# Kernel tuning notes

Hardware: AMD Instinct MI355X
Metric: run time of the kernel (lower is better)

The kernel has to match this reference:

```python
import jax, jax.numpy as jnp
import numpy as np
import math

NTOKEN = 32000; D = 512; H = 8; DFF = 2048; L = 4; B = 4; S = 1024; EPS = 1e-5


def _ln(x, g, b):
    m = x.mean(-1, keepdims=True)
    v = ((x - m) ** 2).mean(-1, keepdims=True)
    return (x - m) * jax.lax.rsqrt(v + EPS) * g + b


def setup_inputs() -> dict:
    key = jax.random.key(0)
    ks = jax.random.split(key, 20)
    s = 0.02
    rn = lambda k, shape: jax.random.normal(k, shape, jnp.float32) * s
    return {
        "src": jax.random.randint(ks[0], (B, S), 0, NTOKEN, jnp.int32),
        "emb": rn(ks[1], (NTOKEN, D)),
        "conv_w": rn(ks[2], (D, 1, 3)), "conv_b": rn(ks[3], (D,)),
        "bn_g": jnp.ones((D,)), "bn_b": jnp.zeros((D,)),
        "bn_m": jnp.zeros((D,)), "bn_v": jnp.ones((D,)),
        "w_ih": rn(ks[4], (4 * D, D)), "w_hh": rn(ks[5], (4 * D, D)),
        "b_ih": rn(ks[6], (4 * D,)), "b_hh": rn(ks[7], (4 * D,)),
        "in_w": rn(ks[8], (L, 3 * D, D)), "in_b": rn(ks[9], (L, 3 * D)),
        "out_w": rn(ks[10], (L, D, D)), "out_b": rn(ks[11], (L, D)),
        "ln1_g": jnp.ones((L, D)), "ln1_b": jnp.zeros((L, D)),
        "w1": rn(ks[12], (L, DFF, D)), "b1": rn(ks[13], (L, DFF)),
        "w2": rn(ks[14], (L, D, DFF)), "b2": rn(ks[15], (L, D)),
        "ln2_g": jnp.ones((L, D)), "ln2_b": jnp.zeros((L, D)),
        "fin_g": jnp.ones((D,)), "fin_b": jnp.zeros((D,)),
    }


def _forward(src, emb, conv_w, conv_b, bn_g, bn_b, bn_m, bn_v,
             w_ih, w_hh, b_ih, b_hh, in_w, in_b, out_w, out_b,
             ln1_g, ln1_b, w1, b1, w2, b2, ln2_g, ln2_b, fin_g, fin_b):
    d = emb.shape[1]
    x = emb[src] * math.sqrt(d)  # [B,S,D]
    # sinusoidal positional encoding (dropout is identity at eval)
    pos = jnp.arange(S, dtype=jnp.float32)[:, None]
    div = jnp.exp(jnp.arange(0, d, 2, dtype=jnp.float32) * (-math.log(10000.0) / d))
    pe = jnp.zeros((S, d), jnp.float32)
    pe = pe.at[:, 0::2].set(jnp.sin(pos * div)).at[:, 1::2].set(jnp.cos(pos * div))
    x = x + pe[None]
    # depthwise conv k=3 + BatchNorm1d (eval stats) + ReLU
    xc = jnp.transpose(x, (0, 2, 1))  # [B,D,S]
    xc = jax.lax.conv_general_dilated(xc, conv_w, (1,), [(1, 1)],
                                      feature_group_count=d,
                                      dimension_numbers=('NCH', 'OIH', 'NCH'))
    xc = xc + conv_b[None, :, None]
    xc = (xc - bn_m[None, :, None]) * jax.lax.rsqrt(bn_v + EPS)[None, :, None] \
         * bn_g[None, :, None] + bn_b[None, :, None]
    x = jnp.transpose(jax.nn.relu(xc), (0, 2, 1))
    # single-layer LSTM (torch gate order i,f,g,o)
    def step(carry, xt):
        h, c = carry
        gates = xt @ w_ih.T + b_ih + h @ w_hh.T + b_hh
        i, f, g, o = jnp.split(gates, 4, axis=-1)
        c = jax.nn.sigmoid(f) * c + jax.nn.sigmoid(i) * jnp.tanh(g)
        h = jax.nn.sigmoid(o) * jnp.tanh(c)
        return (h, c), h
    h0 = jnp.zeros((x.shape[0], d), x.dtype)
    _, hs = jax.lax.scan(step, (h0, h0), jnp.transpose(x, (1, 0, 2)))
    x = x + jnp.transpose(hs, (1, 0, 2))
    # post-norm encoder layers, attn weights averaged over heads
    hd = d // H
    scale = 1.0 / math.sqrt(hd)
    attns = []
    out = x
    for l in range(L):
        qkv = out @ in_w[l].T + in_b[l]
        q, k, v = jnp.split(qkv, 3, axis=-1)
        q = q.reshape(B, S, H, hd).transpose(0, 2, 1, 3) * scale
        k = k.reshape(B, S, H, hd).transpose(0, 2, 1, 3)
        v = v.reshape(B, S, H, hd).transpose(0, 2, 1, 3)
        a = jax.nn.softmax(jnp.einsum('bhqd,bhkd->bhqk', q, k), axis=-1)
        attns.append(a.mean(axis=1))  # averaged over heads, as need_weights=True default
        ctx = jnp.einsum('bhqk,bhkd->bhqd', a, v).transpose(0, 2, 1, 3).reshape(B, S, d)
        out = _ln(out + ctx @ out_w[l].T + out_b[l], ln1_g[l], ln1_b[l])
        ff = jax.nn.gelu(out @ w1[l].T + b1[l], approximate=False) @ w2[l].T + b2[l]
        out = _ln(out + ff, ln2_g[l], ln2_b[l])
    return _ln(out, fin_g, fin_b), jnp.stack(attns)


def reference(src, emb, conv_w, conv_b, bn_g, bn_b, bn_m, bn_v,
              w_ih, w_hh, b_ih, b_hh, in_w, in_b, out_w, out_b,
              ln1_g, ln1_b, w1, b1, w2, b2, ln2_g, ln2_b, fin_g, fin_b):
    return _forward(src, emb, conv_w, conv_b, bn_g, bn_b, bn_m, bn_v,
                    w_ih, w_hh, b_ih, b_hh, in_w, in_b, out_w, out_b,
                    ln1_g, ln1_b, w1, b1, w2, b2, ln2_g, ln2_b, fin_g, fin_b)
```

## Files before the change

### kernel.cpp

```cpp
#include <hip/hip_runtime.h>
#include <math.h>

#define DD 512
#define SS 1024
#define BB 4
#define HH 8
#define DFF 2048
#define LL 4
#define NT 4096
#define EPSF 1e-5f

#define O_X0    ((size_t)0)
#define O_X1    ((size_t)2097152)
#define O_HSEQ  ((size_t)4194304)
#define O_CTX   ((size_t)6293504)
#define O_QKV   ((size_t)8390656)
#define O_BIG   ((size_t)14682112)
#define O_BSUM  ((size_t)31459328)

typedef unsigned int  u32;
typedef unsigned short u16;
typedef __attribute__((ext_vector_type(8))) _Float16 f16x8;
typedef __attribute__((ext_vector_type(4))) _Float16 f16x4;
typedef __attribute__((ext_vector_type(4))) float    f32x4;

__device__ __forceinline__ float fsig(float x){
  return __builtin_amdgcn_rcpf(1.0f + __expf(-x));
}
__device__ __forceinline__ float ftanh(float x){
  return 1.0f - 2.0f*__builtin_amdgcn_rcpf(1.0f + __expf(2.0f*x));
}
struct h2 { _Float16 hi, lo; };
__device__ __forceinline__ h2 split2(float v){
  h2 r; r.hi = (_Float16)v; r.lo = (_Float16)(v - (float)r.hi); return r;
}
union f16u { u16 u; _Float16 f; };
__device__ __forceinline__ float b2f(u16 b){ f16u t; t.u = b; return (float)t.f; }
__device__ __forceinline__ u16 f2b(_Float16 h){ f16u t; t.f = h; return t.u; }
__device__ __forceinline__ u32 pack2(float v){
  _Float16 hi = (_Float16)v;
  _Float16 lo = (_Float16)(v - (float)hi);
  return (u32)f2b(hi) | ((u32)f2b(lo) << 16);
}
__device__ __forceinline__ float unpack2f(u32 w){
  return b2f((u16)w) + b2f((u16)(w >> 16));
}

__global__ void k_embed(const int* __restrict__ src, const float* __restrict__ emb,
                        float* __restrict__ x){
  int idx = blockIdx.x*256 + threadIdx.x;
  if (idx >= NT*DD) return;
  int d = idx & (DD-1);
  int n = idx >> 9;
  int s = n & (SS-1);
  int tok = src[n];
  int i2 = d & ~1;
  float div = expf(-(float)i2 * (9.210340371976184f/512.0f));
  float ang = (float)s * div;
  float pe = (d & 1) ? cosf(ang) : sinf(ang);
  x[idx] = emb[(size_t)tok*DD + d]*22.62741699796952f + pe;
}

__global__ void k_conv(const float* __restrict__ x, const float* __restrict__ cw,
                       const float* __restrict__ cb, const float* __restrict__ bg,
                       const float* __restrict__ bb, const float* __restrict__ bm,
                       const float* __restrict__ bv, float* __restrict__ y){
  int idx = blockIdx.x*256 + threadIdx.x;
  if (idx >= NT*DD) return;
  int d = idx & (DD-1);
  int n = idx >> 9;
  int s = n & (SS-1);
  float acc = cb[d];
  if (s > 0)     acc += x[idx - DD]*cw[d*3+0];
  acc += x[idx]*cw[d*3+1];
  if (s < SS-1)  acc += x[idx + DD]*cw[d*3+2];
  float v = (acc - bm[d])*rsqrtf(bv[d]+EPSF)*bg[d] + bb[d];
  y[idx] = fmaxf(v, 0.0f);
}

__global__ void k_bsum(const float* a, const float* b, float* o, int n){
  int i = blockIdx.x*256 + threadIdx.x;
  if (i < n) o[i] = a[i] + b[i];
}

template<int QSCALE>
__global__ void k_wsplit(const float* __restrict__ W, u32* __restrict__ Wp,
                         const float* __restrict__ bias_in, float* __restrict__ bias_out,
                         int total, int K){
  int i = blockIdx.x*1024 + threadIdx.x*4;
  if (i < total){
    float4 v = *reinterpret_cast<const float4*>(W + i);
    float s = 1.0f;
    if (QSCALE){ int row = i / K; if (row < 512) s = 0.125f; }
    uint4 o;
    o.x = pack2(v.x*s); o.y = pack2(v.y*s); o.z = pack2(v.z*s); o.w = pack2(v.w*s);
    *reinterpret_cast<uint4*>(Wp + i) = o;
  }
  if (QSCALE && blockIdx.x == 0){
    for (int j = threadIdx.x; j < 1536; j += 256){
      float bv = bias_in[j];
      bias_out[j] = (j < 512) ? bv*0.125f : bv;
    }
  }
}

__global__ void k_asplit(const float* __restrict__ A, u32* __restrict__ Ap, int total){
  int i = blockIdx.x*1024 + threadIdx.x*4;
  if (i >= total) return;
  float4 v = *reinterpret_cast<const float4*>(A + i);
  uint4 o;
  o.x = pack2(v.x); o.y = pack2(v.y); o.z = pack2(v.z); o.w = pack2(v.w);
  *reinterpret_cast<uint4*>(Ap + i) = o;
}

__device__ __forceinline__ void unpk4(uint4 w, uint2& hi, uint2& lo){
  hi.x = (w.x & 0xffffu) | (w.y << 16);
  hi.y = (w.z & 0xffffu) | (w.w << 16);
  lo.x = (w.x >> 16) | (w.y & 0xffff0000u);
  lo.y = (w.z >> 16) | (w.w & 0xffff0000u);
}

#define BKP 40
template<int ACT, int APRE, int OSPLIT>
__global__ __launch_bounds__(256) void k_gemm_mfma(const void* __restrict__ Ain,
                                                   const u32* __restrict__ Wp,
                                                   const float* __restrict__ bias,
                                                   void* __restrict__ Cout,
                                                   int M, int N, int K){
  __shared__ _Float16 Ah[128][BKP];
  __shared__ _Float16 Al[128][BKP];
  __shared__ _Float16 Wh[128][BKP];
  __shared__ _Float16 Wl[128][BKP];
  const int tid = threadIdx.x;
  const int nbx = N >> 7;
  const int bx = blockIdx.x % nbx;
  const int by = blockIdx.x / nbx;
  const int m0 = by << 7, n0 = bx << 7;
  const int lane = tid & 63;
  const int wid  = tid >> 6;
  const int wr = wid >> 1, wc = wid & 1;
  const int fm = lane & 15, fg = lane >> 4;
  const int r0 = tid >> 3;
  const int k4 = (tid & 7) << 2;
  const u32* Wbase = Wp + (size_t)(n0 + r0)*K + k4;

  f32x4 acc[4][4];
  #pragma unroll
  for (int i=0;i<4;i++)
    #pragma unroll
    for (int j=0;j<4;j++) acc[i][j] = (f32x4){0.0f,0.0f,0.0f,0.0f};

  uint4 rw[4];
  uint4 ra4[4];
  float4 raf[4];
  #pragma unroll
  for (int e=0;e<4;e++)
    rw[e] = *reinterpret_cast<const uint4*>(Wbase + (size_t)(e*32)*K);
  if constexpr (APRE){
    const u32* Abase = (const u32*)Ain + (size_t)(m0 + r0)*K + k4;
    #pragma unroll
    for (int e=0;e<4;e++)
      ra4[e] = *reinterpret_cast<const uint4*>(Abase + (size_t)(e*32)*K);
  } else {
    const float* Abase = (const float*)Ain + (size_t)(m0 + r0)*K + k4;
    #pragma unroll
    for (int e=0;e<4;e++)
      raf[e] = *reinterpret_cast<const float4*>(Abase + (size_t)(e*32)*K);
  }

  for (int k0 = 0; k0 < K; k0 += 32){
    #pragma unroll
    for (int e = 0; e < 4; ++e){
      int rr = r0 + e*32;
      uint2 hi, lo;
      unpk4(rw[e], hi, lo);
      *reinterpret_cast<uint2*>(&Wh[rr][k4]) = hi;
      *reinterpret_cast<uint2*>(&Wl[rr][k4]) = lo;
      if constexpr (APRE){
        unpk4(ra4[e], hi, lo);
        *reinterpret_cast<uint2*>(&Ah[rr][k4]) = hi;
        *reinterpret_cast<uint2*>(&Al[rr][k4]) = lo;
      } else {
        f16x4 ahv, alv;
        h2 t;
        t = split2(raf[e].x); ahv[0]=t.hi; alv[0]=t.lo;
        t = split2(raf[e].y); ahv[1]=t.hi; alv[1]=t.lo;
        t = split2(raf[e].z); ahv[2]=t.hi; alv[2]=t.lo;
        t = split2(raf[e].w); ahv[3]=t.hi; alv[3]=t.lo;
        *reinterpret_cast<f16x4*>(&Ah[rr][k4]) = ahv;
        *reinterpret_cast<f16x4*>(&Al[rr][k4]) = alv;
      }
    }
    __syncthreads();
    if (k0 + 32 < K){
      #pragma unroll
      for (int e=0;e<4;e++)
        rw[e] = *reinterpret_cast<const uint4*>(Wbase + (size_t)(e*32)*K + k0 + 32);
      if constexpr (APRE){
        const u32* Abase = (const u32*)Ain + (size_t)(m0 + r0)*K + k4;
        #pragma unroll
        for (int e=0;e<4;e++)
          ra4[e] = *reinterpret_cast<const uint4*>(Abase + (size_t)(e*32)*K + k0 + 32);
      } else {
        const float* Abase = (const float*)Ain + (size_t)(m0 + r0)*K + k4;
        #pragma unroll
        for (int e=0;e<4;e++)
          raf[e] = *reinterpret_cast<const float4*>(Abase + (size_t)(e*32)*K + k0 + 32);
      }
    }
    f16x8 a_h[4], a_l[4], w_h[4], w_l[4];
    #pragma unroll
    for (int i=0;i<4;i++){
      int row = wr*64 + i*16 + fm;
      a_h[i] = *reinterpret_cast<const f16x8*>(&Ah[row][fg*8]);
      a_l[i] = *reinterpret_cast<const f16x8*>(&Al[row][fg*8]);
    }
    #pragma unroll
    for (int j=0;j<4;j++){
      int row = wc*64 + j*16 + fm;
      w_h[j] = *reinterpret_cast<const f16x8*>(&Wh[row][fg*8]);
      w_l[j] = *reinterpret_cast<const f16x8*>(&Wl[row][fg*8]);
    }
    #pragma unroll
    for (int i=0;i<4;i++)
      #pragma unroll
      for (int j=0;j<4;j++){
        acc[i][j] = __builtin_amdgcn_mfma_f32_16x16x32_f16(a_h[i], w_h[j], acc[i][j], 0, 0, 0);
        acc[i][j] = __builtin_amdgcn_mfma_f32_16x16x32_f16(a_h[i], w_l[j], acc[i][j], 0, 0, 0);
        acc[i][j] = __builtin_amdgcn_mfma_f32_16x16x32_f16(a_l[i], w_h[j], acc[i][j], 0, 0, 0);
      }
    __syncthreads();
  }
  #pragma unroll
  for (int i=0;i<4;i++){
    #pragma unroll
    for (int r=0;r<4;r++){
      int row = m0 + wr*64 + i*16 + fg*4 + r;
      #pragma unroll
      for (int j=0;j<4;j++){
        int col = n0 + wc*64 + j*16 + fm;
        float v = acc[i][j][r] + bias[col];
        if (ACT == 1) v = 0.5f*v*(1.0f + erff(v*0.70710678118654752f));
        if constexpr (OSPLIT) ((u32*)Cout)[(size_t)row*N + col] = pack2(v);
        else                  ((float*)Cout)[(size_t)row*N + col] = v;
      }
    }
  }
}

#define SPAD 72
__global__ __launch_bounds__(256) void k_scores_mfma(const u32* __restrict__ qkv,
                                                     u32* __restrict__ sc, int bbase){
  __shared__ _Float16 Qh[128][SPAD], Ql[128][SPAD];
  __shared__ _Float16 Kh[128][SPAD], Kl[128][SPAD];
  const int tid = threadIdx.x;
  const int kt = blockIdx.x & 7;
  const int qt = (blockIdx.x >> 3) & 7;
  const int h  = (blockIdx.x >> 6) & 7;
  const int hb = (blockIdx.x >> 9) & 1;
  const int b  = bbase + hb;
  const int q0 = qt*128, k0 = kt*128;
  #pragma unroll
  for (int e=0;e<8;e++){
    int lin = e*256 + tid;
    int rr = lin >> 4;
    int c4 = (lin & 15) << 2;
    uint4 qv = *reinterpret_cast<const uint4*>(qkv + (size_t)(b*SS + q0+rr)*1536 + h*64 + c4);
    uint4 kv = *reinterpret_cast<const uint4*>(qkv + (size_t)(b*SS + k0+rr)*1536 + DD + h*64 + c4);
    uint2 hi, lo;
    unpk4(qv, hi, lo);
    *reinterpret_cast<uint2*>(&Qh[rr][c4]) = hi;
    *reinterpret_cast<uint2*>(&Ql[rr][c4]) = lo;
    unpk4(kv, hi, lo);
    *reinterpret_cast<uint2*>(&Kh[rr][c4]) = hi;
    *reinterpret_cast<uint2*>(&Kl[rr][c4]) = lo;
  }
  __syncthreads();
  const int lane = tid & 63, wid = tid >> 6;
  const int wr = wid >> 1, wc = wid & 1;
  const int fm = lane & 15, fg = lane >> 4;
  f32x4 acc[4][4];
  #pragma unroll
  for (int i=0;i<4;i++)
    #pragma unroll
    for (int j=0;j<4;j++) acc[i][j] = (f32x4){0.0f,0.0f,0.0f,0.0f};
  #pragma unroll
  for (int ks=0; ks<2; ks++){
    f16x8 ah[4], al[4], bh[4], bl[4];
    #pragma unroll
    for (int i=0;i<4;i++){
      int row = wr*64 + i*16 + fm;
      ah[i] = *reinterpret_cast<const f16x8*>(&Qh[row][ks*32 + fg*8]);
      al[i] = *reinterpret_cast<const f16x8*>(&Ql[row][ks*32 + fg*8]);
    }
    #pragma unroll
    for (int j=0;j<4;j++){
      int row = wc*64 + j*16 + fm;
      bh[j] = *reinterpret_cast<const f16x8*>(&Kh[row][ks*32 + fg*8]);
      bl[j] = *reinterpret_cast<const f16x8*>(&Kl[row][ks*32 + fg*8]);
    }
    #pragma unroll
    for (int i=0;i<4;i++)
      #pragma unroll
      for (int j=0;j<4;j++){
        acc[i][j] = __builtin_amdgcn_mfma_f32_16x16x32_f16(ah[i], bh[j], acc[i][j], 0, 0, 0);
        acc[i][j] = __builtin_amdgcn_mfma_f32_16x16x32_f16(ah[i], bl[j], acc[i][j], 0, 0, 0);
        acc[i][j] = __builtin_amdgcn_mfma_f32_16x16x32_f16(al[i], bh[j], acc[i][j], 0, 0, 0);
      }
  }
  u32* out = sc + (size_t)(hb*HH + h)*SS*SS;
  #pragma unroll
  for (int i=0;i<4;i++){
    #pragma unroll
    for (int r=0;r<4;r++){
      int row = q0 + wr*64 + i*16 + fg*4 + r;
      #pragma unroll
      for (int j=0;j<4;j++){
        int col = k0 + wc*64 + j*16 + fm;
        out[(size_t)row*SS + col] = pack2(acc[i][j][r]);
      }
    }
  }
}

__global__ __launch_bounds__(256) void k_pv_mfma(const u32* __restrict__ sc,
                                                 const u32* __restrict__ qkv,
                                                 float* __restrict__ ctx, int bbase){
  __shared__ _Float16 Ph[128][SPAD];
  __shared__ _Float16 Vh[64][SPAD],  Vl[64][SPAD];
  const int tid = threadIdx.x;
  const int qt = blockIdx.x & 7;
  const int h  = (blockIdx.x >> 3) & 7;
  const int hb = (blockIdx.x >> 6) & 1;
  const int b  = bbase + hb;
  const int q0 = qt*128;
  const u16* Pb = (const u16*)(sc + (size_t)(hb*HH + h)*SS*SS);
  const int lane = tid & 63, wid = tid >> 6;
  const int wr = wid >> 1, wc = wid & 1;
  const int fm = lane & 15, fg = lane >> 4;
  const int pr0 = tid >> 4;
  const int pc4 = (tid & 15) << 2;
  const int vd  = tid & 63;
  const int vk0 = tid >> 6;
  const u16* Pbase = Pb + (size_t)(q0 + pr0)*2*SS + pc4;
  const u32* Vbase = qkv + (size_t)(b*SS + vk0)*1536 + 1024 + h*64 + vd;
  f32x4 acc[4][2];
  #pragma unroll
  for (int i=0;i<4;i++){ acc[i][0] = (f32x4){0,0,0,0}; acc[i][1] = (f32x4){0,0,0,0}; }

  uint2 rp[8];
  u32   rv[16];
  #pragma unroll
  for (int e=0;e<8;e++)  rp[e] = *reinterpret_cast<const uint2*>(Pbase + (size_t)(e*16)*2*SS);
  #pragma unroll
  for (int e=0;e<16;e++) rv[e] = Vbase[(size_t)(e*4)*1536];

  for (int kk0=0; kk0<SS; kk0+=64){
    #pragma unroll
    for (int e=0;e<8;e++){
      int rr = pr0 + e*16;
      *reinterpret_cast<uint2*>(&Ph[rr][pc4]) = rp[e];
    }
    #pragma unroll
    for (int e=0;e<16;e++){
      int k = vk0 + e*4;
      u32 w = rv[e];
      f16u thi, tlo; thi.u = (u16)w; tlo.u = (u16)(w >> 16);
      Vh[vd][k] = thi.f;
      Vl[vd][k] = tlo.f;
    }
    __syncthreads();
    if (kk0 + 64 < SS){
      #pragma unroll
      for (int e=0;e<8;e++)
        rp[e] = *reinterpret_cast<const uint2*>(Pbase + (size_t)(e*16)*2*SS + kk0 + 64);
      #pragma unroll
      for (int e=0;e<16;e++)
        rv[e] = Vbase[(size_t)(kk0 + 64 + e*4)*1536];
    }
    #pragma unroll
    for (int ks=0; ks<2; ks++){
      f16x8 ah[4], bh[2], bl[2];
      #pragma unroll
      for (int i=0;i<4;i++){
        int row = wr*64 + i*16 + fm;
        ah[i] = *reinterpret_cast<const f16x8*>(&Ph[row][ks*32 + fg*8]);
      }
      #pragma unroll
      for (int j=0;j<2;j++){
        int row = wc*32 + j*16 + fm;
        bh[j] = *reinterpret_cast<const f16x8*>(&Vh[row][ks*32 + fg*8]);
        bl[j] = *reinterpret_cast<const f16x8*>(&Vl[row][ks*32 + fg*8]);
      }
      #pragma unroll
      for (int i=0;i<4;i++)
        #pragma unroll
        for (int j=0;j<2;j++){
          acc[i][j] = __builtin_amdgcn_mfma_f32_16x16x32_f16(ah[i], bh[j], acc[i][j], 0, 0, 0);
          acc[i][j] = __builtin_amdgcn_mfma_f32_16x16x32_f16(ah[i], bl[j], acc[i][j], 0, 0, 0);
        }
    }
    __syncthreads();
  }
  #pragma unroll
  for (int i=0;i<4;i++){
    #pragma unroll
    for (int r=0;r<4;r++){
      int row = q0 + wr*64 + i*16 + fg*4 + r;
      #pragma unroll
      for (int j=0;j<2;j++){
        int col = wc*32 + j*16 + fm;
        ctx[(size_t)(b*SS + row)*DD + h*64 + col] = acc[i][j][r];
      }
    }
  }
}

__global__ __launch_bounds__(256) void k_lstm(const float* __restrict__ gates_in,
                                              const float* __restrict__ w_hh,
                                              unsigned long long* __restrict__ hpack){
  __shared__ float hsh[2][DD];
  const int b = blockIdx.x >> 6;
  const int chunk = blockIdx.x & 63;
  const int d0 = chunk*8;
  const int tid = threadIdx.x;
  const int wave = tid >> 6;
  const int lane = tid & 63;
  const int diw = lane >> 5;
  const int g   = (lane >> 3) & 3;
  const int ks  = lane & 7;
  const int dim = wave*2 + diw;
  const int src0 = diw*32;
  float w[64];
  {
    const float* wrow = w_hh + (size_t)(g*DD + d0 + dim)*DD;
    #pragma unroll
    for (int j=0;j<64;j++) w[j] = wrow[j*8 + ks];
  }
  float c = 0.0f;
  const float* gbase = gates_in + (size_t)(b*SS)*(4*DD) + g*DD + d0 + dim;
  unsigned long long p0 = __hip_atomic_load(hpack + (size_t)b*DD + tid,
                                            __ATOMIC_RELAXED, __HIP_MEMORY_SCOPE_AGENT);
  unsigned long long p1 = __hip_atomic_load(hpack + (size_t)b*DD + tid + 256,
                                            __ATOMIC_RELAXED, __HIP_MEMORY_SCOPE_AGENT);
  for (int t=0; t<SS; ++t){
    float gv = 0.0f;
    if (ks == 0) gv = gbase[(size_t)t*(4*DD)];
    const unsigned long long exp_tag = (unsigned long long)t;
    unsigned long long* hp = hpack + (size_t)(t*BB + b)*DD;
    while ((p0 >> 32) != exp_tag || (p1 >> 32) != exp_tag){
      if ((p0 >> 32) != exp_tag)
        p0 = __hip_atomic_load(hp + tid,       __ATOMIC_RELAXED, __HIP_MEMORY_SCOPE_AGENT);
      if ((p1 >> 32) != exp_tag)
        p1 = __hip_atomic_load(hp + tid + 256, __ATOMIC_RELAXED, __HIP_MEMORY_SCOPE_AGENT);
    }
    float* hs = hsh[t & 1];
    union { unsigned int u; float f; } u0, u1;
    u0.u = (unsigned int)p0;
    u1.u = (unsigned int)p1;
    hs[tid]       = u0.f;
    hs[tid + 256] = u1.f;
    __syncthreads();
    if (t + 1 < SS){
      unsigned long long* hq = hpack + (size_t)((t+1)*BB + b)*DD;
      p0 = __hip_atomic_load(hq + tid,       __ATOMIC_RELAXED, __HIP_MEMORY_SCOPE_AGENT);
      p1 = __hip_atomic_load(hq + tid + 256, __ATOMIC_RELAXED, __HIP_MEMORY_SCOPE_AGENT);
    }
    float a0=0.0f, a1=0.0f, a2=0.0f, a3=0.0f;
    #pragma unroll
    for (int j=0;j<64;j+=4){
      a0 += w[j+0]*hs[(j+0)*8 + ks];
      a1 += w[j+1]*hs[(j+1)*8 + ks];
      a2 += w[j+2]*hs[(j+2)*8 + ks];
      a3 += w[j+3]*hs[(j+3)*8 + ks];
    }
    float acc = (a0+a1)+(a2+a3);
    acc += __shfl_down(acc, 4, 8);
    acc += __shfl_down(acc, 2, 8);
    acc += __shfl_down(acc, 1, 8);
    float v = acc + gv;
    float gval = (g == 2) ? ftanh(v) : fsig(v);
    float gi = __shfl(gval, src0 + 0);
    float gf = __shfl(gval, src0 + 8);
    float gg = __shfl(gval, src0 + 16);
    float go = __shfl(gval, src0 + 24);
    c = gf*c + gi*gg;
    float h = go*ftanh(c);
    if (lane == src0){
      union { float f; unsigned int u; } hu; hu.f = h;
      unsigned long long pk = ((unsigned long long)(unsigned int)(t+1) << 32)
                            | (unsigned long long)hu.u;
      __hip_atomic_store(&hpack[(size_t)((t+1)*BB + b)*DD + d0 + dim], pk,
                         __ATOMIC_RELAXED, __HIP_MEMORY_SCOPE_AGENT);
    }
  }
}

__global__ void k_resid(float* __restrict__ x, const unsigned long long* __restrict__ hpack){
  int idx = blockIdx.x*256 + threadIdx.x;
  if (idx >= NT*DD) return;
  int d = idx & (DD-1);
  int n = idx >> 9;
  int s = n & (SS-1);
  int b = n >> 10;
  union { unsigned int u; float f; } hu;
  hu.u = (unsigned int)hpack[(size_t)((s+1)*BB + b)*DD + d];
  x[idx] += hu.f;
}

__global__ __launch_bounds__(256) void k_softmax(u32* __restrict__ sc,
                                                 float* __restrict__ attn_out,
                                                 int l, int bbase){
  __shared__ float avgw[4][SS];
  const int tid = threadIdx.x;
  const int q  = blockIdx.x & (SS-1);
  const int hb = blockIdx.x >> 10;
  const int b = bbase + hb;
  const int wave = tid >> 6, lane = tid & 63;
  #pragma unroll
  for (int j=0;j<16;j++) avgw[wave][j*64 + lane] = 0.0f;
  #pragma unroll
  for (int hi=0; hi<2; hi++){
    int h = wave + hi*4;
    u32* row = sc + (size_t)(hb*HH + h)*SS*SS + (size_t)q*SS;
    float v[16];
    float m = -1e30f;
    #pragma unroll
    for (int j=0;j<16;j++){ v[j] = unpack2f(row[j*64 + lane]); m = fmaxf(m, v[j]); }
    #pragma unroll
    for (int o=32;o>0;o>>=1) m = fmaxf(m, __shfl_xor(m, o));
    float s = 0.0f;
    #pragma unroll
    for (int j=0;j<16;j++){ v[j] = __expf(v[j] - m); s += v[j]; }
    #pragma unroll
    for (int o=32;o>0;o>>=1) s += __shfl_xor(s, o);
    float inv = __builtin_amdgcn_rcpf(s);
    u16* p16 = (u16*)row;
    #pragma unroll
    for (int j=0;j<16;j++){
      float p = v[j]*inv;
      p16[j*64 + lane] = f2b((_Float16)p);
      avgw[wave][j*64 + lane] += p;
    }
  }
  __syncthreads();
  float* ao = attn_out + (size_t)((l*BB + b)*SS + q)*SS;
  for (int j=tid;j<SS;j+=256)
    ao[j] = (avgw[0][j]+avgw[1][j]+avgw[2][j]+avgw[3][j])*0.125f;
}

__global__ __launch_bounds__(64) void k_ln(const float* __restrict__ x,
                                           const float* __restrict__ y,
                                           const float* __restrict__ g,
                                           const float* __restrict__ bta,
                                           float* __restrict__ out){
  const int n = blockIdx.x;
  const int tid = threadIdx.x;
  float v[8];
  float s = 0.0f, sq = 0.0f;
  #pragma unroll
  for (int j=0;j<8;j++){
    int d = j*64 + tid;
    float a = x[(size_t)n*DD + d];
    if (y) a += y[(size_t)n*DD + d];
    v[j] = a; s += a; sq += a*a;
  }
  #pragma unroll
  for (int o=32;o>0;o>>=1){ s += __shfl_xor(s, o); sq += __shfl_xor(sq, o); }
  float mean = s*(1.0f/DD);
  float var = sq*(1.0f/DD) - mean*mean;
  float rstd = rsqrtf(var + EPSF);
  #pragma unroll
  for (int j=0;j<8;j++){
    int d = j*64 + tid;
    out[(size_t)n*DD + d] = (v[j]-mean)*rstd*g[d] + bta[d];
  }
}

extern "C" void kernel_launch(void* const* d_in, const int* in_sizes, int n_in,
                              void* d_out, int out_size, void* d_ws, size_t ws_size,
                              hipStream_t stream){
  const int*   src    = (const int*)  d_in[0];
  const float* emb    = (const float*)d_in[1];
  const float* conv_w = (const float*)d_in[2];
  const float* conv_b = (const float*)d_in[3];
  const float* bn_g   = (const float*)d_in[4];
  const float* bn_b   = (const float*)d_in[5];
  const float* bn_m   = (const float*)d_in[6];
  const float* bn_v   = (const float*)d_in[7];
  const float* w_ih   = (const float*)d_in[8];
  const float* w_hh   = (const float*)d_in[9];
  const float* b_ih   = (const float*)d_in[10];
  const float* b_hh   = (const float*)d_in[11];
  const float* in_w   = (const float*)d_in[12];
  const float* in_b   = (const float*)d_in[13];
  const float* out_w  = (const float*)d_in[14];
  const float* out_b  = (const float*)d_in[15];
  const float* ln1_g  = (const float*)d_in[16];
  const float* ln1_b  = (const float*)d_in[17];
  const float* w1     = (const float*)d_in[18];
  const float* b1     = (const float*)d_in[19];
  const float* w2     = (const float*)d_in[20];
  const float* b2     = (const float*)d_in[21];
  const float* ln2_g  = (const float*)d_in[22];
  const float* ln2_b  = (const float*)d_in[23];
  const float* fin_g  = (const float*)d_in[24];
  const float* fin_b  = (const float*)d_in[25];

  float* ws    = (float*)d_ws;
  float* x0    = ws + O_X0;
  float* x1    = ws + O_X1;
  float* ctx   = ws + O_CTX;
  float* qkv   = ws + O_QKV;
  float* big   = ws + O_BIG;
  float* bsum  = ws + O_BSUM;
  unsigned long long* hpack = (unsigned long long*)(big + 8388608);

  u32*   aconv = (u32*)(ws + O_HSEQ);
  float* qbias = ws + O_HSEQ + 2097152;
  u32*   qkvp  = (u32*)qkv;
  u32*   scp   = (u32*)big;
  u32*   wsg   = (u32*)(big + 13000000);
  u32*   wsa   = (u32*)big;
  u32*   ws1   = (u32*)(big + 8500000);
  u32*   ws2   = (u32*)(big + 9500000);

  float* outx  = (float*)d_out;
  float* attn  = outx + (size_t)NT*DD;

  hipMemsetAsync(hpack, 0, (size_t)(SS+1)*BB*DD*sizeof(unsigned long long), stream);

  const int eb = (NT*DD)/256;
  k_embed<<<eb, 256, 0, stream>>>(src, emb, x0);
  k_conv <<<eb, 256, 0, stream>>>(x0, conv_w, conv_b, bn_g, bn_b, bn_m, bn_v, x1);
  k_bsum <<<8, 256, 0, stream>>>(b_ih, b_hh, bsum, 4*DD);

  k_asplit<<<2048, 256, 0, stream>>>(x1, aconv, NT*DD);
  k_wsplit<0><<<1024, 256, 0, stream>>>(w_ih, wsg, nullptr, nullptr, 2048*512, 512);
  k_gemm_mfma<0,1,0><<<(NT/128)*((4*DD)/128), 256, 0, stream>>>(
      aconv, wsg, bsum, big, NT, 4*DD, DD);
  k_lstm<<<256, 256, 0, stream>>>(big, w_hh, hpack);
  k_resid<<<eb, 256, 0, stream>>>(x1, hpack);

  float* cur = x1;
  float* tmp = x0;
  for (int l=0; l<LL; ++l){
    k_asplit<<<2048, 256, 0, stream>>>(cur, aconv, NT*DD);
    k_wsplit<1><<<768, 256, 0, stream>>>(in_w + (size_t)l*1536*DD, wsa,
                                         in_b + (size_t)l*1536, qbias, 1536*512, 512);
    k_gemm_mfma<0,1,1><<<(NT/128)*(1536/128), 256, 0, stream>>>(
        aconv, wsa, qbias, qkvp, NT, 1536, DD);
    for (int bb2=0; bb2<2; ++bb2){
      int bbase = bb2*2;
      k_scores_mfma<<<1024, 256, 0, stream>>>(qkvp, scp, bbase);
      k_softmax    <<<2048, 256, 0, stream>>>(scp, attn, l, bbase);
      k_pv_mfma    <<<128,  256, 0, stream>>>(scp, qkvp, ctx, bbase);
    }
    k_wsplit<0><<<256, 256, 0, stream>>>(out_w + (size_t)l*DD*DD, wsa,
                                         nullptr, nullptr, 512*512, 512);
    k_gemm_mfma<0,0,0><<<(NT/128)*(DD/128), 256, 0, stream>>>(
        ctx, wsa, out_b + (size_t)l*DD, tmp, NT, DD, DD);
    k_ln<<<NT, 64, 0, stream>>>(cur, tmp, ln1_g + l*DD, ln1_b + l*DD, cur);
    k_asplit<<<2048, 256, 0, stream>>>(cur, aconv, NT*DD);
    k_wsplit<0><<<1024, 256, 0, stream>>>(w1 + (size_t)l*DFF*DD, ws1,
                                          nullptr, nullptr, 2048*512, 512);
    k_gemm_mfma<1,1,1><<<(NT/128)*(DFF/128), 256, 0, stream>>>(
        aconv, ws1, b1 + (size_t)l*DFF, (u32*)big, NT, DFF, DD);
    k_wsplit<0><<<1024, 256, 0, stream>>>(w2 + (size_t)l*DD*DFF, ws2,
                                          nullptr, nullptr, 512*2048, 2048);
    k_gemm_mfma<0,1,0><<<(NT/128)*(DD/128), 256, 0, stream>>>(
        (u32*)big, ws2, b2 + (size_t)l*DD, tmp, NT, DD, DFF);
    k_ln<<<NT, 64, 0, stream>>>(cur, tmp, ln2_g + l*DD, ln2_b + l*DD, cur);
  }
  k_ln<<<NT, 64, 0, stream>>>(cur, nullptr, fin_g, fin_b, outx);
}
```

Baseline: 2.922 ms.

## Fuse fp16 split packing into producers, retile PV, transpose LSTM hidden smem

Removes the standalone k_asplit passes by having the conv, residual and layernorm kernels also write the packed hi/lo fp16 copy of their output. This saves a full read and write of the activation tensor before each GEMM. k_pv_mfma is retiled to 64-row query tiles, so it launches twice as many blocks (256 instead of 128) for better CU occupancy. The LSTM hidden-state shared buffer is transposed and padded so each thread reads a contiguous float4, which reduces LDS bank conflicts in the serial recurrence.

New measurement: 2.775 ms. 1.05x faster.

```diff
diff --git a/kernel.cpp b/kernel.cpp
--- a/kernel.cpp
+++ b/kernel.cpp
@@ -64,7 +64,8 @@
 __global__ void k_conv(const float* __restrict__ x, const float* __restrict__ cw,
                        const float* __restrict__ cb, const float* __restrict__ bg,
                        const float* __restrict__ bb, const float* __restrict__ bm,
-                       const float* __restrict__ bv, float* __restrict__ y){
+                       const float* __restrict__ bv, float* __restrict__ y,
+                       u32* __restrict__ yp){
   int idx = blockIdx.x*256 + threadIdx.x;
   if (idx >= NT*DD) return;
   int d = idx & (DD-1);
@@ -75,7 +76,9 @@
   acc += x[idx]*cw[d*3+1];
   if (s < SS-1)  acc += x[idx + DD]*cw[d*3+2];
   float v = (acc - bm[d])*rsqrtf(bv[d]+EPSF)*bg[d] + bb[d];
-  y[idx] = fmaxf(v, 0.0f);
+  v = fmaxf(v, 0.0f);
+  y[idx] = v;
+  yp[idx] = pack2(v);
 }
 
 __global__ void k_bsum(const float* a, const float* b, float* o, int n){
@@ -102,15 +105,6 @@
       bias_out[j] = (j < 512) ? bv*0.125f : bv;
     }
   }
-}
-
-__global__ void k_asplit(const float* __restrict__ A, u32* __restrict__ Ap, int total){
-  int i = blockIdx.x*1024 + threadIdx.x*4;
-  if (i >= total) return;
-  float4 v = *reinterpret_cast<const float4*>(A + i);
-  uint4 o;
-  o.x = pack2(v.x); o.y = pack2(v.y); o.z = pack2(v.z); o.w = pack2(v.w);
-  *reinterpret_cast<uint4*>(Ap + i) = o;
 }
 
 __device__ __forceinline__ void unpk4(uint4 w, uint2& hi, uint2& lo){
@@ -326,14 +320,14 @@
 __global__ __launch_bounds__(256) void k_pv_mfma(const u32* __restrict__ sc,
                                                  const u32* __restrict__ qkv,
                                                  float* __restrict__ ctx, int bbase){
-  __shared__ _Float16 Ph[128][SPAD];
+  __shared__ _Float16 Ph[64][SPAD];
   __shared__ _Float16 Vh[64][SPAD],  Vl[64][SPAD];
   const int tid = threadIdx.x;
-  const int qt = blockIdx.x & 7;
-  const int h  = (blockIdx.x >> 3) & 7;
-  const int hb = (blockIdx.x >> 6) & 1;
+  const int qt = blockIdx.x & 15;
+  const int h  = (blockIdx.x >> 4) & 7;
+  const int hb = (blockIdx.x >> 7) & 1;
   const int b  = bbase + hb;
-  const int q0 = qt*128;
+  const int q0 = qt*64;
   const u16* Pb = (const u16*)(sc + (size_t)(hb*HH + h)*SS*SS);
   const int lane = tid & 63, wid = tid >> 6;
   const int wr = wid >> 1, wc = wid & 1;
@@ -344,20 +338,20 @@
   const int vk0 = tid >> 6;
   const u16* Pbase = Pb + (size_t)(q0 + pr0)*2*SS + pc4;
   const u32* Vbase = qkv + (size_t)(b*SS + vk0)*1536 + 1024 + h*64 + vd;
-  f32x4 acc[4][2];
-  #pragma unroll
-  for (int i=0;i<4;i++){ acc[i][0] = (f32x4){0,0,0,0}; acc[i][1] = (f32x4){0,0,0,0}; }
-
-  uint2 rp[8];
+  f32x4 acc[2][2];
+  #pragma unroll
+  for (int i=0;i<2;i++){ acc[i][0] = (f32x4){0,0,0,0}; acc[i][1] = (f32x4){0,0,0,0}; }
+
+  uint2 rp[4];
   u32   rv[16];
   #pragma unroll
-  for (int e=0;e<8;e++)  rp[e] = *reinterpret_cast<const uint2*>(Pbase + (size_t)(e*16)*2*SS);
+  for (int e=0;e<4;e++)  rp[e] = *reinterpret_cast<const uint2*>(Pbase + (size_t)(e*16)*2*SS);
   #pragma unroll
   for (int e=0;e<16;e++) rv[e] = Vbase[(size_t)(e*4)*1536];
 
   for (int kk0=0; kk0<SS; kk0+=64){
     #pragma unroll
-    for (int e=0;e<8;e++){
+    for (int e=0;e<4;e++){
       int rr = pr0 + e*16;
       *reinterpret_cast<uint2*>(&Ph[rr][pc4]) = rp[e];
     }
@@ -372,7 +366,7 @@
     __syncthreads();
     if (kk0 + 64 < SS){
       #pragma unroll
-      for (int e=0;e<8;e++)
+      for (int e=0;e<4;e++)
         rp[e] = *reinterpret_cast<const uint2*>(Pbase + (size_t)(e*16)*2*SS + kk0 + 64);
       #pragma unroll
       for (int e=0;e<16;e++)
@@ -380,10 +374,10 @@
     }
     #pragma unroll
     for (int ks=0; ks<2; ks++){
-      f16x8 ah[4], bh[2], bl[2];
-      #pragma unroll
-      for (int i=0;i<4;i++){
-        int row = wr*64 + i*16 + fm;
+      f16x8 ah[2], bh[2], bl[2];
+      #pragma unroll
+      for (int i=0;i<2;i++){
+        int row = wr*32 + i*16 + fm;
         ah[i] = *reinterpret_cast<const f16x8*>(&Ph[row][ks*32 + fg*8]);
       }
       #pragma unroll
@@ -393,7 +387,7 @@
         bl[j] = *reinterpret_cast<const f16x8*>(&Vl[row][ks*32 + fg*8]);
       }
       #pragma unroll
-      for (int i=0;i<4;i++)
+      for (int i=0;i<2;i++)
         #pragma unroll
         for (int j=0;j<2;j++){
           acc[i][j] = __builtin_amdgcn_mfma_f32_16x16x32_f16(ah[i], bh[j], acc[i][j], 0, 0, 0);
@@ -403,10 +397,10 @@
     __syncthreads();
   }
   #pragma unroll
-  for (int i=0;i<4;i++){
+  for (int i=0;i<2;i++){
     #pragma unroll
     for (int r=0;r<4;r++){
-      int row = q0 + wr*64 + i*16 + fg*4 + r;
+      int row = q0 + wr*32 + i*16 + fg*4 + r;
       #pragma unroll
       for (int j=0;j<2;j++){
         int col = wc*32 + j*16 + fm;
@@ -419,7 +413,7 @@
 __global__ __launch_bounds__(256) void k_lstm(const float* __restrict__ gates_in,
                                               const float* __restrict__ w_hh,
                                               unsigned long long* __restrict__ hpack){
-  __shared__ float hsh[2][DD];
+  __shared__ float hsh[2][8][68];
   const int b = blockIdx.x >> 6;
   const int chunk = blockIdx.x & 63;
   const int d0 = chunk*8;
@@ -454,12 +448,12 @@
       if ((p1 >> 32) != exp_tag)
         p1 = __hip_atomic_load(hp + tid + 256, __ATOMIC_RELAXED, __HIP_MEMORY_SCOPE_AGENT);
     }
-    float* hs = hsh[t & 1];
+    float (*hs)[68] = hsh[t & 1];
     union { unsigned int u; float f; } u0, u1;
     u0.u = (unsigned int)p0;
     u1.u = (unsigned int)p1;
-    hs[tid]       = u0.f;
-    hs[tid + 256] = u1.f;
+    hs[tid & 7][tid >> 3]        = u0.f;
+    hs[tid & 7][(tid >> 3) + 32] = u1.f;
     __syncthreads();
     if (t + 1 < SS){
       unsigned long long* hq = hpack + (size_t)((t+1)*BB + b)*DD;
@@ -469,10 +463,11 @@
     float a0=0.0f, a1=0.0f, a2=0.0f, a3=0.0f;
     #pragma unroll
     for (int j=0;j<64;j+=4){
-      a0 += w[j+0]*hs[(j+0)*8 + ks];
-      a1 += w[j+1]*hs[(j+1)*8 + ks];
-      a2 += w[j+2]*hs[(j+2)*8 + ks];
-      a3 += w[j+3]*hs[(j+3)*8 + ks];
+      float4 hv = *reinterpret_cast<const float4*>(&hs[ks][j]);
+      a0 += w[j+0]*hv.x;
+      a1 += w[j+1]*hv.y;
+      a2 += w[j+2]*hv.z;
+      a3 += w[j+3]*hv.w;
     }
     float acc = (a0+a1)+(a2+a3);
     acc += __shfl_down(acc, 4, 8);
@@ -496,7 +491,8 @@
   }
 }
 
-__global__ void k_resid(float* __restrict__ x, const unsigned long long* __restrict__ hpack){
+__global__ void k_resid(float* __restrict__ x, const unsigned long long* __restrict__ hpack,
+                        u32* __restrict__ xp){
   int idx = blockIdx.x*256 + threadIdx.x;
   if (idx >= NT*DD) return;
   int d = idx & (DD-1);
@@ -505,7 +501,9 @@
   int b = n >> 10;
   union { unsigned int u; float f; } hu;
   hu.u = (unsigned int)hpack[(size_t)((s+1)*BB + b)*DD + d];
-  x[idx] += hu.f;
+  float v = x[idx] + hu.f;
+  x[idx] = v;
+  xp[idx] = pack2(v);
 }
 
 __global__ __launch_bounds__(256) void k_softmax(u32* __restrict__ sc,
@@ -553,7 +551,8 @@
                                            const float* __restrict__ y,
                                            const float* __restrict__ g,
                                            const float* __restrict__ bta,
-                                           float* __restrict__ out){
+                                           float* __restrict__ out,
+                                           u32* __restrict__ outp){
   const int n = blockIdx.x;
   const int tid = threadIdx.x;
   float v[8];
@@ -573,7 +572,9 @@
   #pragma unroll
   for (int j=0;j<8;j++){
     int d = j*64 + tid;
-    out[(size_t)n*DD + d] = (v[j]-mean)*rstd*g[d] + bta[d];
+    float r = (v[j]-mean)*rstd*g[d] + bta[d];
+    out[(size_t)n*DD + d] = r;
+    if (outp) outp[(size_t)n*DD + d] = pack2(r);
   }
 }
 
@@ -632,20 +633,18 @@
 
   const int eb = (NT*DD)/256;
   k_embed<<<eb, 256, 0, stream>>>(src, emb, x0);
-  k_conv <<<eb, 256, 0, stream>>>(x0, conv_w, conv_b, bn_g, bn_b, bn_m, bn_v, x1);
+  k_conv <<<eb, 256, 0, stream>>>(x0, conv_w, conv_b, bn_g, bn_b, bn_m, bn_v, x1, aconv);
   k_bsum <<<8, 256, 0, stream>>>(b_ih, b_hh, bsum, 4*DD);
 
-  k_asplit<<<2048, 256, 0, stream>>>(x1, aconv, NT*DD);
   k_wsplit<0><<<1024, 256, 0, stream>>>(w_ih, wsg, nullptr, nullptr, 2048*512, 512);
   k_gemm_mfma<0,1,0><<<(NT/128)*((4*DD)/128), 256, 0, stream>>>(
       aconv, wsg, bsum, big, NT, 4*DD, DD);
   k_lstm<<<256, 256, 0, stream>>>(big, w_hh, hpack);
-  k_resid<<<eb, 256, 0, stream>>>(x1, hpack);
+  k_resid<<<eb, 256, 0, stream>>>(x1, hpack, aconv);
 
   float* cur = x1;
   float* tmp = x0;
   for (int l=0; l<LL; ++l){
-    k_asplit<<<2048, 256, 0, stream>>>(cur, aconv, NT*DD);
     k_wsplit<1><<<768, 256, 0, stream>>>(in_w + (size_t)l*1536*DD, wsa,
                                          in_b + (size_t)l*1536, qbias, 1536*512, 512);
     k_gemm_mfma<0,1,1><<<(NT/128)*(1536/128), 256, 0, stream>>>(
@@ -654,14 +653,13 @@
       int bbase = bb2*2;
       k_scores_mfma<<<1024, 256, 0, stream>>>(qkvp, scp, bbase);
       k_softmax    <<<2048, 256, 0, stream>>>(scp, attn, l, bbase);
-      k_pv_mfma    <<<128,  256, 0, stream>>>(scp, qkvp, ctx, bbase);
+      k_pv_mfma    <<<256,  256, 0, stream>>>(scp, qkvp, ctx, bbase);
     }
     k_wsplit<0><<<256, 256, 0, stream>>>(out_w + (size_t)l*DD*DD, wsa,
                                          nullptr, nullptr, 512*512, 512);
     k_gemm_mfma<0,0,0><<<(NT/128)*(DD/128), 256, 0, stream>>>(
         ctx, wsa, out_b + (size_t)l*DD, tmp, NT, DD, DD);
-    k_ln<<<NT, 64, 0, stream>>>(cur, tmp, ln1_g + l*DD, ln1_b + l*DD, cur);
-    k_asplit<<<2048, 256, 0, stream>>>(cur, aconv, NT*DD);
+    k_ln<<<NT, 64, 0, stream>>>(cur, tmp, ln1_g + l*DD, ln1_b + l*DD, cur, aconv);
     k_wsplit<0><<<1024, 256, 0, stream>>>(w1 + (size_t)l*DFF*DD, ws1,
                                           nullptr, nullptr, 2048*512, 512);
     k_gemm_mfma<1,1,1><<<(NT/128)*(DFF/128), 256, 0, stream>>>(
@@ -670,7 +668,7 @@
                                           nullptr, nullptr, 512*2048, 2048);
     k_gemm_mfma<0,1,0><<<(NT/128)*(DD/128), 256, 0, stream>>>(
         (u32*)big, ws2, b2 + (size_t)l*DD, tmp, NT, DD, DFF);
-    k_ln<<<NT, 64, 0, stream>>>(cur, tmp, ln2_g + l*DD, ln2_b + l*DD, cur);
-  }
-  k_ln<<<NT, 64, 0, stream>>>(cur, nullptr, fin_g, fin_b, outx);
-}
+    k_ln<<<NT, 64, 0, stream>>>(cur, tmp, ln2_g + l*DD, ln2_b + l*DD, cur, aconv);
+  }
+  k_ln<<<NT, 64, 0, stream>>>(cur, nullptr, fin_g, fin_b, outx, nullptr);
+}
```
